# Optimization experiments

Measured on AMD Instinct MI355X. Metric: run time of the kernel, lower is better.

## Reference

```python
import jax, jax.numpy as jnp
import numpy as np

RADIUS = 9.0
GROUPS = 4
BLK = 64  # row block for streaming the N x N pairwise convolution


def leaky(x):
    return jnp.where(x >= 0, x, 0.2 * x)


def group_norm(x, gamma, beta, eps=1e-5):
    # x: (N, C); matches torch.nn.GroupNorm(GROUPS, C) applied to (1, C, N)
    N, C = x.shape
    xg = x.T.reshape(GROUPS, (C // GROUPS) * N)
    m = xg.mean(axis=1, keepdims=True)
    v = ((xg - m) ** 2).mean(axis=1, keepdims=True)
    xg = (xg - m) / jnp.sqrt(v + eps)
    return xg.reshape(C, N).T * gamma + beta


def tangent_vectors(n):
    # Duff et al. orthonormal tangent basis; n: (N,3) unit normals -> (N,2,3)
    x, y, z = n[:, 0], n[:, 1], n[:, 2]
    s = jnp.where(z >= 0, 1.0, -1.0)
    a = -1.0 / (s + z)
    b = x * y * a
    uv = jnp.stack([1 + s * x * x * a, s * b, -s * x, b, s + y * y * a, -y], axis=-1)
    return uv.reshape(-1, 2, 3)


def load_mesh(xyz, normals, weights):
    # Build oriented local frames nuv (N,3,3) as in dMaSIFConv_seg.load_mesh
    p = xyz / RADIUS
    uv = tangent_vectors(normals)                  # (N,2,3)
    diff = p[None, :, :] - p[:, None, :]           # (N,N,3): x_j - x_i
    d2 = jnp.sum(diff * diff, axis=-1)             # (N,N)
    cos = normals @ normals.T                      # (N,N)
    window = jnp.exp(-d2 * (2.0 - cos) ** 2)       # pseudo-geodesic Gaussian
    X = jnp.einsum('ikd,ijd->ijk', uv, diff)       # (N,N,2) tangent coords
    ov = jnp.einsum('ij,j,ijk->ik', window, weights[:, 0], X) + 1e-5  # (N,2)
    nrm = jnp.maximum(jnp.linalg.norm(ov, axis=-1, keepdims=True), 1e-12)
    ov = ov / nrm                                  # F.normalize
    ex, ey = ov[:, :1], ov[:, 1:]
    u, v = uv[:, 0, :], uv[:, 1, :]
    return jnp.stack([normals, ex * u + ey * v, -ey * u + ex * v], axis=1)


def dmasif_conv(points, nuv, feats,
                ni_w1, ni_b1, ni_w2, ni_b2, gn_in_g, gn_in_b,
                cv_a1, cv_b1, cv_a2, cv_b2,
                no_w1, no_b1, no_w2, no_b2, gn_out_g, gn_out_b):
    N = points.shape[0]
    H = ni_w1.shape[0]
    O = no_w1.shape[0]
    # net_in + GroupNorm
    h = leaky(feats @ ni_w1.T + ni_b1)
    h = leaky(h @ ni_w2.T + ni_b2)
    h = group_norm(h, gn_in_g, gn_in_b)            # (N,H)
    p = points / (np.sqrt(2.0) * RADIUS)
    n = jax.lax.stop_gradient(nuv[:, 0, :])        # normals detached in window

    p_blk = p.reshape(-1, BLK, 3)
    n_blk = n.reshape(-1, BLK, 3)
    nuv_blk = nuv.reshape(-1, BLK, 3, 3)

    @jax.checkpoint
    def step(carry, blk):
        pi, ni, nuvi = blk                                  # (B,3),(B,3),(B,3,3)
        diff = p[None, :, :] - pi[:, None, :]               # (B,N,3)
        d2 = jnp.sum(diff * diff, axis=-1)                  # (B,N)
        window = jnp.exp(-d2 * (2.0 - ni @ n.T) ** 2)       # (B,N)
        X = jnp.einsum('bkd,bnd->bnk', nuvi, diff)          # (B,N,3) local coords
        g = jax.nn.relu(jnp.einsum('bnk,ck->bnc', X, cv_a1) + cv_b1)  # (B,N,8)
        M = jax.nn.relu(jnp.einsum('bnc,fc->bnf', g, cv_a2) + cv_b2)  # (B,N,H*O)
        M = M.reshape(BLK, N, O, H)
        out = jnp.einsum('bn,bnoh,nh->bo', window, M, h)    # (B,O)
        return carry, out

    _, outs = jax.lax.scan(step, None, (p_blk, n_blk, nuv_blk))
    y = outs.reshape(N, O)
    y = leaky(y @ no_w1.T + no_b1)
    y = leaky(y @ no_w2.T + no_b2)
    return group_norm(y, gn_out_g, gn_out_b)


def setup_inputs() -> dict:
    key = jax.random.key(0)
    ks = jax.random.split(key, 32)
    N, I, U, H, O, C = 4096, 16, 16, 16, 16, 8
    nrm = jax.random.normal(ks[1], (N, 3), dtype=jnp.float32)
    nrm = nrm / jnp.linalg.norm(nrm, axis=-1, keepdims=True)
    w = lambda k, sh: 0.1 * jax.random.normal(k, sh, dtype=jnp.float32)
    return {
        'surface_xyz': 10.0 * jax.random.normal(ks[0], (N, 3), dtype=jnp.float32),
        'surface_normals': nrm,
        'features': jax.random.normal(ks[2], (N, I), dtype=jnp.float32),
        'os_w1': w(ks[3], (U, I)), 'os_b1': w(ks[4], (U,)),
        'os_w2': w(ks[5], (1, U)), 'os_b2': w(ks[6], (1,)),
        'ni_w1': w(ks[7], (H, I)), 'ni_b1': w(ks[8], (H,)),
        'ni_w2': w(ks[9], (H, H)), 'ni_b2': w(ks[10], (H,)),
        'gn_in_g': jnp.ones((H,), jnp.float32), 'gn_in_b': jnp.zeros((H,), jnp.float32),
        'cv_a1': w(ks[11], (C, 3)), 'cv_b1': w(ks[12], (C,)),
        'cv_a2': w(ks[13], (H * O, C)), 'cv_b2': w(ks[14], (H * O,)),
        'no_w1': w(ks[15], (O, H)), 'no_b1': w(ks[16], (O,)),
        'no_w2': w(ks[17], (O, O)), 'no_b2': w(ks[18], (O,)),
        'gn_out_g': jnp.ones((O,), jnp.float32), 'gn_out_b': jnp.zeros((O,), jnp.float32),
        'll_w1': w(ks[19], (O, O)), 'll_b1': w(ks[20], (O,)),
        'll_w2': w(ks[21], (O, O)), 'll_b2': w(ks[22], (O,)),
        'lt_w': w(ks[23], (O, I)), 'lt_b': w(ks[24], (O,)),
    }


def reference(surface_xyz, surface_normals, features,
              os_w1, os_b1, os_w2, os_b2,
              ni_w1, ni_b1, ni_w2, ni_b2, gn_in_g, gn_in_b,
              cv_a1, cv_b1, cv_a2, cv_b2,
              no_w1, no_b1, no_w2, no_b2, gn_out_g, gn_out_b,
              ll_w1, ll_b1, ll_w2, ll_b2, lt_w, lt_b):
    # orientation scores: Linear -> LeakyReLU(0.2) -> Linear
    scores = leaky(features @ os_w1.T + os_b1) @ os_w2.T + os_b2  # (N,1)
    nuv = load_mesh(surface_xyz, surface_normals, scores)
    # dMaSIFConv_seg forward, n_layers = 1
    x_i = dmasif_conv(surface_xyz, nuv, features,
                      ni_w1, ni_b1, ni_w2, ni_b2, gn_in_g, gn_in_b,
                      cv_a1, cv_b1, cv_a2, cv_b2,
                      no_w1, no_b1, no_w2, no_b2, gn_out_g, gn_out_b)
    x_i = jax.nn.relu(x_i @ ll_w1.T + ll_b1) @ ll_w2.T + ll_b2  # linear_layers[0]
    x = features @ lt_w.T + lt_b                                 # linear_transform[0]
    return x + x_i
```

## Files before the change

kernel.cpp:

```cpp
#include <hip/hip_runtime.h>

#define NP 4096
#define NJC 16
#define JCH (NP / NJC)
#define HR  12

typedef const float* fp;

using half8  = __attribute__((ext_vector_type(8))) _Float16;
using fp16x2 = __attribute__((ext_vector_type(2))) __fp16;
using f32x4  = __attribute__((ext_vector_type(4))) float;

__device__ __forceinline__ float lk(float x) { return x >= 0.f ? x : 0.2f * x; }

__device__ __forceinline__ unsigned int pkrtz(float a, float b) {
    fp16x2 h = __builtin_amdgcn_cvt_pkrtz(a, b);
    unsigned int u; __builtin_memcpy(&u, &h, 4); return u;
}
__device__ __forceinline__ fp16x2 u2h(unsigned int u) {
    fp16x2 h; __builtin_memcpy(&h, &u, 4); return h;
}

#define OFF_ACC   0
#define OFF_OV    16
#define OFF_CONV  (16 + 2*NP)
#define ZERO_FLTS (16 + 2*NP + 16*NP)
#define OFF_SC    ZERO_FLTS
#define OFF_UV    (OFF_SC  + NP)
#define OFF_P9    (OFF_UV  + 6*NP)
#define OFF_NRM   (OFF_P9  + 3*NP)
#define OFF_HPRE  (OFF_NRM + 3*NP)
#define OFF_HNRM  (OFF_HPRE+ 16*NP)
#define OFF_NUV   (OFF_HNRM+ 16*NP)
#define OFF_Y2    (OFF_NUV + 9*NP)
#define WS_FLTS   (OFF_Y2  + 16*NP)

__global__ __launch_bounds__(256) void k_prep(
    fp xyz, fp nrm, fp feats,
    fp osw1, fp osb1, fp osw2, fp osb2,
    fp niw1, fp nib1, fp niw2, fp nib2,
    float* __restrict__ ws)
{
    const int i = blockIdx.x * 256 + threadIdx.x;

    float f[16];
#pragma unroll
    for (int c = 0; c < 16; c++) f[c] = feats[i * 16 + c];

    float sc = osb2[0];
#pragma unroll
    for (int u = 0; u < 16; u++) {
        float a = osb1[u];
#pragma unroll
        for (int c = 0; c < 16; c++) a += osw1[u * 16 + c] * f[c];
        sc += osw2[u] * lk(a);
    }
    ws[OFF_SC + i] = sc;

    float h1[16];
#pragma unroll
    for (int u = 0; u < 16; u++) {
        float a = nib1[u];
#pragma unroll
        for (int c = 0; c < 16; c++) a += niw1[u * 16 + c] * f[c];
        h1[u] = lk(a);
    }
    float h2[16];
#pragma unroll
    for (int u = 0; u < 16; u++) {
        float a = nib2[u];
#pragma unroll
        for (int c = 0; c < 16; c++) a += niw2[u * 16 + c] * h1[c];
        h2[u] = lk(a);
        ws[OFF_HPRE + i * 16 + u] = h2[u];
    }

#pragma unroll
    for (int g = 0; g < 4; g++) {
        float s = 0.f, ss = 0.f;
#pragma unroll
        for (int k = 0; k < 4; k++) { float v = h2[g * 4 + k]; s += v; ss += v * v; }
#pragma unroll
        for (int off = 32; off > 0; off >>= 1) {
            s  += __shfl_down(s,  off);
            ss += __shfl_down(ss, off);
        }
        if ((threadIdx.x & 63) == 0) {
            atomicAdd(&ws[OFF_ACC + g],     s);
            atomicAdd(&ws[OFF_ACC + 4 + g], ss);
        }
    }

    float nx = nrm[i * 3], ny = nrm[i * 3 + 1], nz = nrm[i * 3 + 2];
    float s  = (nz >= 0.f) ? 1.f : -1.f;
    float a  = -1.f / (s + nz);
    float b  = nx * ny * a;
    float ux = 1.f + s * nx * nx * a, uy = s * b,            uz = -s * nx;
    float vx = b,                     vy = s + ny * ny * a,  vz = -ny;
    ws[OFF_UV + i * 6 + 0] = ux; ws[OFF_UV + i * 6 + 1] = uy; ws[OFF_UV + i * 6 + 2] = uz;
    ws[OFF_UV + i * 6 + 3] = vx; ws[OFF_UV + i * 6 + 4] = vy; ws[OFF_UV + i * 6 + 5] = vz;
    const float IR = 1.f / 9.f;
    ws[OFF_P9 + i * 3 + 0] = xyz[i * 3 + 0] * IR;
    ws[OFF_P9 + i * 3 + 1] = xyz[i * 3 + 1] * IR;
    ws[OFF_P9 + i * 3 + 2] = xyz[i * 3 + 2] * IR;
    ws[OFF_NRM + i * 3 + 0] = nx;
    ws[OFF_NRM + i * 3 + 1] = ny;
    ws[OFF_NRM + i * 3 + 2] = nz;
}

__global__ __launch_bounds__(256) void k_mesh(float* __restrict__ ws)
{
    __shared__ float sp[3][512];
    __shared__ float sn[3][512];
    __shared__ float ssc[512];
    __shared__ float red[256][2];

    const int tid = threadIdx.x;
    const int ib = blockIdx.x >> 3, jc = blockIdx.x & 7;
    const int il = tid & 63, sub = tid >> 6;
    const int i = ib * 64 + il;
    const int j0 = jc * 512;

    for (int t = tid; t < 512; t += 256) {
        int j = j0 + t;
        sp[0][t] = ws[OFF_P9 + j * 3];     sp[1][t] = ws[OFF_P9 + j * 3 + 1];  sp[2][t] = ws[OFF_P9 + j * 3 + 2];
        sn[0][t] = ws[OFF_NRM + j * 3];    sn[1][t] = ws[OFF_NRM + j * 3 + 1]; sn[2][t] = ws[OFF_NRM + j * 3 + 2];
        ssc[t]   = ws[OFF_SC + j];
    }
    __syncthreads();

    const float pix = ws[OFF_P9 + i * 3], piy = ws[OFF_P9 + i * 3 + 1], piz = ws[OFF_P9 + i * 3 + 2];
    const float nix = ws[OFF_NRM + i * 3], niy = ws[OFF_NRM + i * 3 + 1], niz = ws[OFF_NRM + i * 3 + 2];
    const float ux = ws[OFF_UV + i * 6],     uy = ws[OFF_UV + i * 6 + 1], uz = ws[OFF_UV + i * 6 + 2];
    const float vx = ws[OFF_UV + i * 6 + 3], vy = ws[OFF_UV + i * 6 + 4], vz = ws[OFF_UV + i * 6 + 5];

    float ov0 = 0.f, ov1 = 0.f;
#pragma unroll 4
    for (int t = 0; t < 128; t++) {
        int j = sub * 128 + t;
        float dx = sp[0][j] - pix, dy = sp[1][j] - piy, dz = sp[2][j] - piz;
        float d2 = dx * dx + dy * dy + dz * dz;
        float cs = nix * sn[0][j] + niy * sn[1][j] + niz * sn[2][j];
        float tt = 2.f - cs;
        float w  = __expf(-d2 * tt * tt) * ssc[j];
        ov0 += w * (ux * dx + uy * dy + uz * dz);
        ov1 += w * (vx * dx + vy * dy + vz * dz);
    }
    red[tid][0] = ov0; red[tid][1] = ov1;
    __syncthreads();
    if (sub == 0) {
        float a = ov0 + red[64 + il][0] + red[128 + il][0] + red[192 + il][0];
        float b = ov1 + red[64 + il][1] + red[128 + il][1] + red[192 + il][1];
        atomicAdd(&ws[OFF_OV + i * 2],     a);
        atomicAdd(&ws[OFF_OV + i * 2 + 1], b);
    }
}

__global__ __launch_bounds__(256) void k_fin(float* __restrict__ ws, fp gng, fp gnb)
{
    const int i = blockIdx.x * 256 + threadIdx.x;

    float o0 = ws[OFF_OV + i * 2]     + 1e-5f;
    float o1 = ws[OFF_OV + i * 2 + 1] + 1e-5f;
    float nr = fmaxf(sqrtf(o0 * o0 + o1 * o1), 1e-12f);
    float ex = o0 / nr, ey = o1 / nr;

    const float ux = ws[OFF_UV + i * 6],     uy = ws[OFF_UV + i * 6 + 1], uz = ws[OFF_UV + i * 6 + 2];
    const float vx = ws[OFF_UV + i * 6 + 3], vy = ws[OFF_UV + i * 6 + 4], vz = ws[OFF_UV + i * 6 + 5];
    const float nx = ws[OFF_NRM + i * 3], ny = ws[OFF_NRM + i * 3 + 1], nz = ws[OFF_NRM + i * 3 + 2];

    ws[OFF_NUV + i * 9 + 0] = nx;
    ws[OFF_NUV + i * 9 + 1] = ny;
    ws[OFF_NUV + i * 9 + 2] = nz;
    ws[OFF_NUV + i * 9 + 3] =  ex * ux + ey * vx;
    ws[OFF_NUV + i * 9 + 4] =  ex * uy + ey * vy;
    ws[OFF_NUV + i * 9 + 5] =  ex * uz + ey * vz;
    ws[OFF_NUV + i * 9 + 6] = -ey * ux + ex * vx;
    ws[OFF_NUV + i * 9 + 7] = -ey * uy + ex * vy;
    ws[OFF_NUV + i * 9 + 8] = -ey * uz + ex * vz;

    const float invM = 1.f / (4.f * NP);
#pragma unroll
    for (int c = 0; c < 16; c++) {
        int g = c >> 2;
        float m   = ws[OFF_ACC + g] * invM;
        float var = ws[OFF_ACC + 4 + g] * invM - m * m;
        float inv = rsqrtf(var + 1e-5f);
        ws[OFF_HNRM + i * 16 + c] =
            (ws[OFF_HPRE + i * 16 + c] - m) * inv * gng[c] + gnb[c];
    }
}

__global__ __launch_bounds__(256, 2) void k_conv(
    const float* __restrict__ ws,
    const float* __restrict__ cva1, const float* __restrict__ cvb1,
    const float* __restrict__ A2,   const float* __restrict__ B2,
    float* __restrict__ conv)
{
    __shared__ float4 sP[JCH];
    __shared__ float4 sN[JCH];
    __shared__ __align__(16) unsigned int sH2[JCH * HR];

    const int tid  = threadIdx.x;
    const int ib   = blockIdx.x >> 4;
    const int jc   = blockIdx.x & 15;
    const int j0   = jc * JCH;
    const int lane = tid & 63;
    const int wv   = tid >> 6;
    const int o    = lane & 15;
    const int quad = lane >> 4;
    const float IVS2 = 0.70710678118654752f;

    {
        const int t = tid;
        const int j = j0 + t;
        sP[t] = make_float4(ws[OFF_P9 + j * 3] * IVS2,
                            ws[OFF_P9 + j * 3 + 1] * IVS2,
                            ws[OFF_P9 + j * 3 + 2] * IVS2, 0.f);
        sN[t] = make_float4(ws[OFF_NRM + j * 3],
                            ws[OFF_NRM + j * 3 + 1],
                            ws[OFF_NRM + j * 3 + 2], 0.f);
        const float4* hs = (const float4*)(ws + OFF_HNRM + j * 16);
        float4 h0 = hs[0], h1 = hs[1], h2 = hs[2], h3 = hs[3];
        uint4 w0, w1;
        w0.x = pkrtz(h0.x, h0.y); w0.y = pkrtz(h0.z, h0.w);
        w0.z = pkrtz(h1.x, h1.y); w0.w = pkrtz(h1.z, h1.w);
        w1.x = pkrtz(h2.x, h2.y); w1.y = pkrtz(h2.z, h2.w);
        w1.z = pkrtz(h3.x, h3.y); w1.w = pkrtz(h3.z, h3.w);
        *(uint4*)(sH2 + t * HR)     = w0;
        *(uint4*)(sH2 + t * HR + 4) = w1;
    }

    const half8 h8z = (half8)(_Float16)0.f;

    half8 Bf[16];
#pragma unroll
    for (int t = 0; t < 16; t++) {
        half8 v = h8z;
        if (lane < 16) {
            const float* row = A2 + (o * 16 + t) * 8;
#pragma unroll
            for (int c = 0; c < 8; c++) v[c] = (_Float16)row[c];
        } else if (lane < 32) {
            v[0] = (_Float16)B2[o * 16 + t];
        }
        Bf[t] = v;
    }

    float a1[24], b1c[8];
#pragma unroll
    for (int k = 0; k < 24; k++) a1[k] = cva1[k];
#pragma unroll
    for (int k = 0; k < 8; k++)  b1c[k] = cvb1[k];

    __syncthreads();

    const f32x4 zc = {0.f, 0.f, 0.f, 0.f};
    const fp16x2 h2z = {(__fp16)0.f, (__fp16)0.f};

#pragma unroll 1
    for (int ii = 0; ii < 16; ii++) {
        const int i = ib * 64 + wv * 16 + ii;
        const float pix = ws[OFF_P9 + i * 3 + 0] * IVS2;
        const float piy = ws[OFF_P9 + i * 3 + 1] * IVS2;
        const float piz = ws[OFF_P9 + i * 3 + 2] * IVS2;
        float r[9];
#pragma unroll
        for (int k = 0; k < 9; k++) r[k] = ws[OFF_NUV + i * 9 + k];

        float accO = 0.f;

#pragma unroll 1
        for (int jg = 0; jg < 4; jg++) {
            const int jl = jg * 64 + lane;
            const float4 pj = sP[jl];
            const float4 nj = sN[jl];
            const float dx = pj.x - pix, dy = pj.y - piy, dz = pj.z - piz;
            const float d2 = dx * dx + dy * dy + dz * dz;
            const float cs = r[0] * nj.x + r[1] * nj.y + r[2] * nj.z;
            const float tt = 2.f - cs;
            const float wwin = __expf(-d2 * tt * tt);
            const float X0 = r[0] * dx + r[1] * dy + r[2] * dz;
            const float X1 = r[3] * dx + r[4] * dy + r[5] * dz;
            const float X2 = r[6] * dx + r[7] * dy + r[8] * dz;
            float g[8];
#pragma unroll
            for (int c = 0; c < 8; c++)
                g[c] = fmaxf(a1[c * 3] * X0 + a1[c * 3 + 1] * X1 +
                             a1[c * 3 + 2] * X2 + b1c[c], 0.f);
            unsigned int wg0 = pkrtz(wwin * g[0], wwin * g[1]);
            unsigned int wg1 = pkrtz(wwin * g[2], wwin * g[3]);
            unsigned int wg2 = pkrtz(wwin * g[4], wwin * g[5]);
            unsigned int wg3 = pkrtz(wwin * g[6], wwin * g[7]);
            unsigned int whp = pkrtz(wwin, 0.f);

#pragma unroll 1
            for (int tau = 0; tau < 4; tau++) {
                const int src = tau * 16 + o;
                unsigned int a0  = (unsigned int)__shfl((int)wg0, src, 64);
                unsigned int a1i = (unsigned int)__shfl((int)wg1, src, 64);
                unsigned int a2i = (unsigned int)__shfl((int)wg2, src, 64);
                unsigned int a3i = (unsigned int)__shfl((int)wg3, src, 64);
                unsigned int aw  = (unsigned int)__shfl((int)whp, src, 64);
                uint4 av;
                av.x = (quad == 0) ? a0 : ((quad == 1) ? aw : 0u);
                av.y = (quad == 0) ? a1i : 0u;
                av.z = (quad == 0) ? a2i : 0u;
                av.w = (quad == 0) ? a3i : 0u;
                half8 Af; __builtin_memcpy(&Af, &av, 16);

                fp16x2 P[32];
#pragma unroll
                for (int q = 0; q < 8; q++) {
                    f32x4 C0 = __builtin_amdgcn_mfma_f32_16x16x32_f16(Af, Bf[2 * q],     zc, 0, 0, 0);
                    f32x4 C1 = __builtin_amdgcn_mfma_f32_16x16x32_f16(Af, Bf[2 * q + 1], zc, 0, 0, 0);
#pragma unroll
                    for (int r2 = 0; r2 < 4; r2++) {
                        fp16x2 pp = __builtin_amdgcn_cvt_pkrtz(C0[r2], C1[r2]);
                        P[r2 * 8 + q] = __builtin_elementwise_max(pp, h2z);
                    }
                }

#pragma unroll
                for (int r2 = 0; r2 < 4; r2++) {
                    const unsigned int* hr = sH2 + (jg * 64 + tau * 16 + quad * 4 + r2) * HR;
                    const uint4 ha = *(const uint4*)hr;
                    const uint4 hb = *(const uint4*)(hr + 4);
                    accO = __builtin_amdgcn_fdot2(P[r2 * 8 + 0], u2h(ha.x), accO, false);
                    accO = __builtin_amdgcn_fdot2(P[r2 * 8 + 1], u2h(ha.y), accO, false);
                    accO = __builtin_amdgcn_fdot2(P[r2 * 8 + 2], u2h(ha.z), accO, false);
                    accO = __builtin_amdgcn_fdot2(P[r2 * 8 + 3], u2h(ha.w), accO, false);
                    accO = __builtin_amdgcn_fdot2(P[r2 * 8 + 4], u2h(hb.x), accO, false);
                    accO = __builtin_amdgcn_fdot2(P[r2 * 8 + 5], u2h(hb.y), accO, false);
                    accO = __builtin_amdgcn_fdot2(P[r2 * 8 + 6], u2h(hb.z), accO, false);
                    accO = __builtin_amdgcn_fdot2(P[r2 * 8 + 7], u2h(hb.w), accO, false);
                }
            }
        }

        accO += __shfl_xor(accO, 16, 64);
        accO += __shfl_xor(accO, 32, 64);
        if (lane < 16) atomicAdd(&conv[i * 16 + o], accO);
    }
}

__global__ __launch_bounds__(256) void k_post1(
    float* __restrict__ ws, fp now1, fp nob1, fp now2, fp nob2)
{
    const int i = blockIdx.x * 256 + threadIdx.x;
    float cv[16];
#pragma unroll
    for (int o = 0; o < 16; o++) cv[o] = ws[OFF_CONV + i * 16 + o];

    float y1[16];
#pragma unroll
    for (int u = 0; u < 16; u++) {
        float a = nob1[u];
#pragma unroll
        for (int k = 0; k < 16; k++) a += now1[u * 16 + k] * cv[k];
        y1[u] = lk(a);
    }
    float y2[16];
#pragma unroll
    for (int u = 0; u < 16; u++) {
        float a = nob2[u];
#pragma unroll
        for (int k = 0; k < 16; k++) a += now2[u * 16 + k] * y1[k];
        y2[u] = lk(a);
        ws[OFF_Y2 + i * 16 + u] = y2[u];
    }
#pragma unroll
    for (int g = 0; g < 4; g++) {
        float s = 0.f, ss = 0.f;
#pragma unroll
        for (int k = 0; k < 4; k++) { float v = y2[g * 4 + k]; s += v; ss += v * v; }
#pragma unroll
        for (int off = 32; off > 0; off >>= 1) {
            s  += __shfl_down(s,  off);
            ss += __shfl_down(ss, off);
        }
        if ((threadIdx.x & 63) == 0) {
            atomicAdd(&ws[OFF_ACC + 8 + g],  s);
            atomicAdd(&ws[OFF_ACC + 12 + g], ss);
        }
    }
}

__global__ __launch_bounds__(256) void k_post2(
    const float* __restrict__ ws, fp feats, fp gg, fp gb,
    fp llw1, fp llb1, fp llw2, fp llb2, fp ltw, fp ltb,
    float* __restrict__ out)
{
    const int i = blockIdx.x * 256 + threadIdx.x;
    const float invM = 1.f / (4.f * NP);

    float z[16];
#pragma unroll
    for (int c = 0; c < 16; c++) {
        int g = c >> 2;
        float m   = ws[OFF_ACC + 8 + g] * invM;
        float var = ws[OFF_ACC + 12 + g] * invM - m * m;
        float inv = rsqrtf(var + 1e-5f);
        z[c] = (ws[OFF_Y2 + i * 16 + c] - m) * inv * gg[c] + gb[c];
    }
    float r1[16];
#pragma unroll
    for (int o = 0; o < 16; o++) {
        float a = llb1[o];
#pragma unroll
        for (int k = 0; k < 16; k++) a += llw1[o * 16 + k] * z[k];
        r1[o] = fmaxf(a, 0.f);
    }
    float f[16];
#pragma unroll
    for (int c = 0; c < 16; c++) f[c] = feats[i * 16 + c];
#pragma unroll
    for (int o = 0; o < 16; o++) {
        float a = llb2[o];
#pragma unroll
        for (int k = 0; k < 16; k++) a += llw2[o * 16 + k] * r1[k];
        float x = ltb[o];
#pragma unroll
        for (int k = 0; k < 16; k++) x += ltw[o * 16 + k] * f[k];
        out[i * 16 + o] = x + a;
    }
}

extern "C" void kernel_launch(void* const* d_in, const int* in_sizes, int n_in,
                              void* d_out, int out_size, void* d_ws, size_t ws_size,
                              hipStream_t stream)
{
    fp xyz  = (fp)d_in[0];
    fp nrm  = (fp)d_in[1];
    fp fts  = (fp)d_in[2];
    fp osw1 = (fp)d_in[3],  osb1 = (fp)d_in[4],  osw2 = (fp)d_in[5],  osb2 = (fp)d_in[6];
    fp niw1 = (fp)d_in[7],  nib1 = (fp)d_in[8],  niw2 = (fp)d_in[9],  nib2 = (fp)d_in[10];
    fp gng  = (fp)d_in[11], gnb  = (fp)d_in[12];
    fp cva1 = (fp)d_in[13], cvb1 = (fp)d_in[14], cva2 = (fp)d_in[15], cvb2 = (fp)d_in[16];
    fp now1 = (fp)d_in[17], nob1 = (fp)d_in[18], now2 = (fp)d_in[19], nob2 = (fp)d_in[20];
    fp gog  = (fp)d_in[21], gob  = (fp)d_in[22];
    fp llw1 = (fp)d_in[23], llb1 = (fp)d_in[24], llw2 = (fp)d_in[25], llb2 = (fp)d_in[26];
    fp ltw  = (fp)d_in[27], ltb  = (fp)d_in[28];

    float* ws = (float*)d_ws;

    (void)hipMemsetAsync(d_ws, 0, (size_t)ZERO_FLTS * sizeof(float), stream);
    k_prep<<<NP / 256, 256, 0, stream>>>(xyz, nrm, fts,
                                         osw1, osb1, osw2, osb2,
                                         niw1, nib1, niw2, nib2, ws);
    k_mesh<<<512, 256, 0, stream>>>(ws);
    k_fin<<<NP / 256, 256, 0, stream>>>(ws, gng, gnb);
    k_conv<<<64 * NJC, 256, 0, stream>>>(ws, cva1, cvb1, cva2, cvb2, ws + OFF_CONV);
    k_post1<<<NP / 256, 256, 0, stream>>>(ws, now1, nob1, now2, nob2);
    k_post2<<<NP / 256, 256, 0, stream>>>(ws, fts, gog, gob,
                                          llw1, llb1, llw2, llb2, ltw, ltb,
                                          (float*)d_out);
}
```

Baseline: 531.1 us.

## Use smaller 16x16x16 MFMA, split j-chunks finer, raise occupancy

Switches the per-pair MLP matmul from the 16x16x32 f16 MFMA with half-empty K to the 16x16x16 variant. The 9-wide input (8 features plus bias) is packed across quads, so fewer padded MACs are issued. The j-range is split into 32 chunks instead of 16, and launch bounds now target 4 blocks per CU. The P buffer is processed in two halves to cut register pressure, and shuffles are replaced by direct ds_bpermute with an inline-asm packed max. Risks are more atomic adds on the output and a host grid size that must match the new NJC, which is not visible here.

```diff
diff --git a/kernel.cpp b/kernel.cpp
--- a/kernel.cpp
+++ b/kernel.cpp
@@ -1,13 +1,13 @@
 #include <hip/hip_runtime.h>
 
 #define NP 4096
-#define NJC 16
+#define NJC 32
 #define JCH (NP / NJC)
 #define HR  12
 
 typedef const float* fp;
 
-using half8  = __attribute__((ext_vector_type(8))) _Float16;
+using half4  = __attribute__((ext_vector_type(4))) __fp16;
 using fp16x2 = __attribute__((ext_vector_type(2))) __fp16;
 using f32x4  = __attribute__((ext_vector_type(4))) float;
 
@@ -19,6 +19,11 @@
 }
 __device__ __forceinline__ fp16x2 u2h(unsigned int u) {
     fp16x2 h; __builtin_memcpy(&h, &u, 4); return h;
+}
+__device__ __forceinline__ fp16x2 pkmax0(fp16x2 a, fp16x2 z) {
+    fp16x2 d;
+    asm("v_pk_max_f16 %0, %1, %2" : "=v"(d) : "v"(a), "v"(z));
+    return d;
 }
 
 #define OFF_ACC   0
@@ -191,7 +196,7 @@
     }
 }
 
-__global__ __launch_bounds__(256, 2) void k_conv(
+__global__ __launch_bounds__(256, 4) void k_conv(
     const float* __restrict__ ws,
     const float* __restrict__ cva1, const float* __restrict__ cvb1,
     const float* __restrict__ A2,   const float* __restrict__ B2,
@@ -202,8 +207,8 @@
     __shared__ __align__(16) unsigned int sH2[JCH * HR];
 
     const int tid  = threadIdx.x;
-    const int ib   = blockIdx.x >> 4;
-    const int jc   = blockIdx.x & 15;
+    const int ib   = blockIdx.x >> 5;
+    const int jc   = blockIdx.x & 31;
     const int j0   = jc * JCH;
     const int lane = tid & 63;
     const int wv   = tid >> 6;
@@ -211,7 +216,7 @@
     const int quad = lane >> 4;
     const float IVS2 = 0.70710678118654752f;
 
-    {
+    if (tid < JCH) {
         const int t = tid;
         const int j = j0 + t;
         sP[t] = make_float4(ws[OFF_P9 + j * 3] * IVS2,
@@ -231,18 +236,19 @@
         *(uint4*)(sH2 + t * HR + 4) = w1;
     }
 
-    const half8 h8z = (half8)(_Float16)0.f;
-
-    half8 Bf[16];
+    half4 Bf[16];
 #pragma unroll
     for (int t = 0; t < 16; t++) {
-        half8 v = h8z;
-        if (lane < 16) {
-            const float* row = A2 + (o * 16 + t) * 8;
-#pragma unroll
-            for (int c = 0; c < 8; c++) v[c] = (_Float16)row[c];
-        } else if (lane < 32) {
-            v[0] = (_Float16)B2[o * 16 + t];
+        half4 v = {(__fp16)0.f, (__fp16)0.f, (__fp16)0.f, (__fp16)0.f};
+        const float* row = A2 + (o * 16 + t) * 8;
+        if (quad == 0) {
+#pragma unroll
+            for (int c = 0; c < 4; c++) v[c] = (__fp16)row[c];
+        } else if (quad == 1) {
+#pragma unroll
+            for (int c = 0; c < 4; c++) v[c] = (__fp16)row[4 + c];
+        } else if (quad == 2) {
+            v[0] = (__fp16)B2[o * 16 + t];
         }
         Bf[t] = v;
     }
@@ -257,6 +263,7 @@
 
     const f32x4 zc = {0.f, 0.f, 0.f, 0.f};
     const fp16x2 h2z = {(__fp16)0.f, (__fp16)0.f};
+    const int o4 = o << 2;
 
 #pragma unroll 1
     for (int ii = 0; ii < 16; ii++) {
@@ -271,7 +278,7 @@
         float accO = 0.f;
 
 #pragma unroll 1
-        for (int jg = 0; jg < 4; jg++) {
+        for (int jg = 0; jg < JCH / 64; jg++) {
             const int jl = jg * 64 + lane;
             const float4 pj = sP[jl];
             const float4 nj = sN[jl];
@@ -288,52 +295,49 @@
             for (int c = 0; c < 8; c++)
                 g[c] = fmaxf(a1[c * 3] * X0 + a1[c * 3 + 1] * X1 +
                              a1[c * 3 + 2] * X2 + b1c[c], 0.f);
-            unsigned int wg0 = pkrtz(wwin * g[0], wwin * g[1]);
-            unsigned int wg1 = pkrtz(wwin * g[2], wwin * g[3]);
-            unsigned int wg2 = pkrtz(wwin * g[4], wwin * g[5]);
-            unsigned int wg3 = pkrtz(wwin * g[6], wwin * g[7]);
-            unsigned int whp = pkrtz(wwin, 0.f);
+            const int wg0 = (int)pkrtz(wwin * g[0], wwin * g[1]);
+            const int wg1 = (int)pkrtz(wwin * g[2], wwin * g[3]);
+            const int wg2 = (int)pkrtz(wwin * g[4], wwin * g[5]);
+            const int wg3 = (int)pkrtz(wwin * g[6], wwin * g[7]);
+            const int whp = (int)pkrtz(wwin, 0.f);
 
 #pragma unroll 1
             for (int tau = 0; tau < 4; tau++) {
-                const int src = tau * 16 + o;
-                unsigned int a0  = (unsigned int)__shfl((int)wg0, src, 64);
-                unsigned int a1i = (unsigned int)__shfl((int)wg1, src, 64);
-                unsigned int a2i = (unsigned int)__shfl((int)wg2, src, 64);
-                unsigned int a3i = (unsigned int)__shfl((int)wg3, src, 64);
-                unsigned int aw  = (unsigned int)__shfl((int)whp, src, 64);
-                uint4 av;
-                av.x = (quad == 0) ? a0 : ((quad == 1) ? aw : 0u);
-                av.y = (quad == 0) ? a1i : 0u;
-                av.z = (quad == 0) ? a2i : 0u;
-                av.w = (quad == 0) ? a3i : 0u;
-                half8 Af; __builtin_memcpy(&Af, &av, 16);
-
-                fp16x2 P[32];
-#pragma unroll
-                for (int q = 0; q < 8; q++) {
-                    f32x4 C0 = __builtin_amdgcn_mfma_f32_16x16x32_f16(Af, Bf[2 * q],     zc, 0, 0, 0);
-                    f32x4 C1 = __builtin_amdgcn_mfma_f32_16x16x32_f16(Af, Bf[2 * q + 1], zc, 0, 0, 0);
+                const int srcb = tau * 64 + o4;
+                const unsigned u0 = (unsigned)__builtin_amdgcn_ds_bpermute(srcb, wg0);
+                const unsigned u1 = (unsigned)__builtin_amdgcn_ds_bpermute(srcb, wg1);
+                const unsigned u2 = (unsigned)__builtin_amdgcn_ds_bpermute(srcb, wg2);
+                const unsigned u3 = (unsigned)__builtin_amdgcn_ds_bpermute(srcb, wg3);
+                const unsigned uw = (unsigned)__builtin_amdgcn_ds_bpermute(srcb, whp);
+                uint2 av;
+                av.x = (quad == 0) ? u0 : (quad == 1) ? u2 : (quad == 2) ? uw : 0u;
+                av.y = (quad == 0) ? u1 : (quad == 1) ? u3 : 0u;
+                half4 Af; __builtin_memcpy(&Af, &av, 8);
+
+#pragma unroll
+                for (int hq = 0; hq < 2; hq++) {
+                    fp16x2 P[16];
+#pragma unroll
+                    for (int q2 = 0; q2 < 4; q2++) {
+                        const int q = hq * 4 + q2;
+                        f32x4 C0 = __builtin_amdgcn_mfma_f32_16x16x16f16(Af, Bf[2 * q],     zc, 0, 0, 0);
+                        f32x4 C1 = __builtin_amdgcn_mfma_f32_16x16x16f16(Af, Bf[2 * q + 1], zc, 0, 0, 0);
+#pragma unroll
+                        for (int r2 = 0; r2 < 4; r2++) {
+                            fp16x2 pp = __builtin_amdgcn_cvt_pkrtz(C0[r2], C1[r2]);
+                            P[r2 * 4 + q2] = pkmax0(pp, h2z);
+                        }
+                    }
 #pragma unroll
                     for (int r2 = 0; r2 < 4; r2++) {
-                        fp16x2 pp = __builtin_amdgcn_cvt_pkrtz(C0[r2], C1[r2]);
-                        P[r2 * 8 + q] = __builtin_elementwise_max(pp, h2z);
+                        const unsigned int* hr =
+                            sH2 + (jg * 64 + tau * 16 + quad * 4 + r2) * HR + hq * 4;
+                        const uint4 ha = *(const uint4*)hr;
+                        accO = __builtin_amdgcn_fdot2(P[r2 * 4 + 0], u2h(ha.x), accO, false);
+                        accO = __builtin_amdgcn_fdot2(P[r2 * 4 + 1], u2h(ha.y), accO, false);
+                        accO = __builtin_amdgcn_fdot2(P[r2 * 4 + 2], u2h(ha.z), accO, false);
+                        accO = __builtin_amdgcn_fdot2(P[r2 * 4 + 3], u2h(ha.w), accO, false);
                     }
-                }
-
-#pragma unroll
-                for (int r2 = 0; r2 < 4; r2++) {
-                    const unsigned int* hr = sH2 + (jg * 64 + tau * 16 + quad * 4 + r2) * HR;
-                    const uint4 ha = *(const uint4*)hr;
-                    const uint4 hb = *(const uint4*)(hr + 4);
-                    accO = __builtin_amdgcn_fdot2(P[r2 * 8 + 0], u2h(ha.x), accO, false);
-                    accO = __builtin_amdgcn_fdot2(P[r2 * 8 + 1], u2h(ha.y), accO, false);
-                    accO = __builtin_amdgcn_fdot2(P[r2 * 8 + 2], u2h(ha.z), accO, false);
-                    accO = __builtin_amdgcn_fdot2(P[r2 * 8 + 3], u2h(ha.w), accO, false);
-                    accO = __builtin_amdgcn_fdot2(P[r2 * 8 + 4], u2h(hb.x), accO, false);
-                    accO = __builtin_amdgcn_fdot2(P[r2 * 8 + 5], u2h(hb.y), accO, false);
-                    accO = __builtin_amdgcn_fdot2(P[r2 * 8 + 6], u2h(hb.z), accO, false);
-                    accO = __builtin_amdgcn_fdot2(P[r2 * 8 + 7], u2h(hb.w), accO, false);
                 }
             }
         }
```

New measurement: 473.6 us. 1.12x faster.
